# Performance work log

Measured on AMD Instinct MI355X. Metric: run time of the kernel, lower is better.

## Reference

```python
import jax, jax.numpy as jnp
from jax import lax
import numpy as np

REG = 0.1        # entropic regularization
ITERS = 50       # Sinkhorn iterations
DS = 8           # avg-pool downsample factor
EPS = 1e-8


def _avg_pool_scaled(x, d):
    # F.avg_pool2d(x, d) * d**2 == sum over non-overlapping dxd windows
    B, C, H, W = x.shape
    return x.reshape(B, C, H // d, d, W // d, d).mean(axis=(3, 5)) * (d * d)


def _cost_matrix(H, W):
    y = jnp.arange(H, dtype=jnp.float32)
    x = jnp.arange(W, dtype=jnp.float32)
    yy, xx = jnp.meshgrid(y, x, indexing='ij')
    coords = jnp.stack([yy.ravel(), xx.ravel()], axis=1)      # [N, 2]
    diff = coords[:, None, :] - coords[None, :, :]            # [N, N, 2]
    return (diff ** 2).sum(axis=-1)                           # [N, N] squared euclidean


def setup_inputs() -> dict:
    key = jax.random.key(0)
    k1, k2 = jax.random.split(key)
    B, H, W = 16, 512, 512
    pred_density = jax.random.uniform(k1, (B, 1, H, W), dtype=jnp.float32)
    gt_density = jax.random.uniform(k2, (B, 1, H, W), dtype=jnp.float32)
    return {"pred_density": pred_density, "gt_density": gt_density}


def reference(pred_density, gt_density):
    pred = _avg_pool_scaled(pred_density, DS)
    gt = _avg_pool_scaled(gt_density, DS)
    B, _, H, W = pred.shape
    N = H * W

    C = _cost_matrix(H, W)          # [N, N]
    K = jnp.exp(-C / REG)           # Gibbs kernel
    M = K * C                       # so cost = u @ (M @ v) == sum(P * C) without materializing P

    a = pred.reshape(B, N)
    b = gt.reshape(B, N)
    a_sum = jnp.clip(a.sum(axis=1), 1e-8, None)
    b_sum = jnp.clip(b.sum(axis=1), 1e-8, None)
    a_n = a / a_sum[:, None]
    b_n = b / b_sum[:, None]

    def sinkhorn_cost(a1, b1):
        def step(carry, _):
            u, v = carry
            v = b1 / (K.T @ u + EPS)
            u = a1 / (K @ v + EPS)
            return (u, v), None
        (u, v), _ = lax.scan(step, (jnp.ones_like(a1), jnp.zeros_like(b1)),
                             None, length=ITERS)
        # P = u[:,None] * K * v[None,:]; (P*C).sum() = u^T (K*C) v
        return u @ (M @ v)

    costs = jax.vmap(sinkhorn_cost)(a_n, b_n)                 # [B]
    valid = (a_sum > 0.5) & (b_sum > 0.5)
    return jnp.where(valid, costs, 0.0).sum() / B
```

## Files before the change

kernel.cpp:

```cpp
#include <hip/hip_runtime.h>


#define G1 4.5399929762484854e-05f
#define EPSF 1e-8f

__device__ __forceinline__ float dpp_shr1(float x) {
  return __int_as_float(__builtin_amdgcn_update_dpp(0, __float_as_int(x), 0x138, 0xF, 0xF, true));
}
__device__ __forceinline__ float dpp_shl1(float x) {
  return __int_as_float(__builtin_amdgcn_update_dpp(0, __float_as_int(x), 0x130, 0xF, 0xF, true));
}

extern "C" __global__ void __launch_bounds__(256)
ot_pool(const float* __restrict__ pred, const float* __restrict__ gt,
        float* __restrict__ ws_pool, double* __restrict__ ws_part) {
  const int bx    = blockIdx.x;
  const int batch = bx & 15;
  const int which = (bx >> 4) & 1;
  const int slice = bx >> 5;
  const float* src  = (which ? gt : pred) + batch * (512 * 512);
  float*       outp = ws_pool + which * (16 * 4096) + batch * 4096;

  double part = 0.0;
  for (int k = 0; k < 2; ++k) {
    const int wi = slice * 512 + k * 256 + threadIdx.x;
    const int y = wi >> 6, x = wi & 63;
    const float* base = src + (y * 8) * 512 + x * 8;
    float s = 0.f;
#pragma unroll
    for (int dy = 0; dy < 8; ++dy) {
      const float4* r4 = (const float4*)(base + dy * 512);
      float4 p0 = r4[0], p1 = r4[1];
      s += ((p0.x + p0.y) + (p0.z + p0.w)) + ((p1.x + p1.y) + (p1.z + p1.w));
    }
    outp[wi] = s;
    part += (double)s;
  }
#pragma unroll
  for (int off = 32; off > 0; off >>= 1) part += __shfl_down(part, off, 64);
  __shared__ double pr[4];
  if ((threadIdx.x & 63) == 0) pr[threadIdx.x >> 6] = part;
  __syncthreads();
  if (threadIdx.x == 0)
    ws_part[slice * 32 + which * 16 + batch] = (pr[0] + pr[1]) + (pr[2] + pr[3]);
}

__device__ __forceinline__ void halfpass(const float (&src)[16], float (&dst)[16],
                                         const float (&wt)[16],
                                         float (*bnd)[4][64], int wv, int lane) {
  float th[16];
#pragma unroll
  for (int r = 0; r < 16; ++r) {
    float l  = dpp_shr1(src[r]);
    float rr = dpp_shl1(src[r]);
    th[r] = __builtin_fmaf(G1, l + rr, src[r]);
  }
  bnd[0][wv][lane] = th[0];
  bnd[1][wv][lane] = th[15];
  __syncthreads();
  float up = (wv > 0) ? bnd[1][wv - 1][lane] : 0.0f;
  float dn = (wv < 3) ? bnd[0][wv + 1][lane] : 0.0f;
#pragma unroll
  for (int r = 1; r < 15; ++r) {
    float s = __builtin_fmaf(G1, th[r - 1] + th[r + 1], th[r]);
    dst[r] = wt[r] * __builtin_amdgcn_rcpf(s + EPSF);
  }
  float s0 = __builtin_fmaf(G1, up + th[1], th[0]);
  dst[0] = wt[0] * __builtin_amdgcn_rcpf(s0 + EPSF);
  float s15 = __builtin_fmaf(G1, th[14] + dn, th[15]);
  dst[15] = wt[15] * __builtin_amdgcn_rcpf(s15 + EPSF);
}

extern "C" __global__ void __launch_bounds__(256)
ot_sinkhorn(const float* __restrict__ ws_pool, const double* __restrict__ ws_part,
            float* __restrict__ ws_cost) {
  const int batch = blockIdx.x;
  const int lane  = threadIdx.x & 63;
  const int wv    = threadIdx.x >> 6;

  __shared__ float  bnd[2][2][4][64];
  __shared__ float  bnd2[4][4][64];
  __shared__ double sums_sh[2];
  __shared__ double red[4];

  if (threadIdx.x == 0) {
    double sa = 0.0, sb = 0.0;
    for (int s = 0; s < 8; ++s) {
      sa += ws_part[s * 32 + batch];
      sb += ws_part[s * 32 + 16 + batch];
    }
    sums_sh[0] = sa; sums_sh[1] = sb;
  }
  __syncthreads();
  const float a_sum = (float)sums_sh[0];
  const float b_sum = (float)sums_sh[1];
  const float inva = 1.0f / fmaxf(a_sum, 1e-8f);
  const float invb = 1.0f / fmaxf(b_sum, 1e-8f);

  float av[16], bv[16], u[16], v[16];
  const float* pa = ws_pool + batch * 4096;
  const float* pb = ws_pool + 16 * 4096 + batch * 4096;
#pragma unroll
  for (int r = 0; r < 16; ++r) {
    const int idx = (wv * 16 + r) * 64 + lane;
    av[r] = pa[idx] * inva;
    bv[r] = pb[idx] * invb;
    u[r]  = 1.0f;
  }

#pragma unroll 1
  for (int it = 0; it < 50; ++it) {
    halfpass(u, v, bv, bnd[0], wv, lane);
    halfpass(v, u, av, bnd[1], wv, lane);
  }

  float tg[16], th2[16];
#pragma unroll
  for (int r = 0; r < 16; ++r) {
    float sh = dpp_shr1(v[r]) + dpp_shl1(v[r]);
    tg[r]  = __builtin_fmaf(G1, sh, v[r]);
    th2[r] = G1 * sh;
  }
  bnd2[0][wv][lane] = tg[0];
  bnd2[1][wv][lane] = tg[15];
  bnd2[2][wv][lane] = th2[0];
  bnd2[3][wv][lane] = th2[15];
  __syncthreads();
  const float tg_up = (wv > 0) ? bnd2[1][wv - 1][lane] : 0.f;
  const float tg_dn = (wv < 3) ? bnd2[0][wv + 1][lane] : 0.f;
  const float th_up = (wv > 0) ? bnd2[3][wv - 1][lane] : 0.f;
  const float th_dn = (wv < 3) ? bnd2[2][wv + 1][lane] : 0.f;

  double acc = 0.0;
#pragma unroll
  for (int r = 0; r < 16; ++r) {
    const float tgm = (r == 0)  ? tg_up : tg[r - 1];
    const float tgp = (r == 15) ? tg_dn : tg[r + 1];
    const float thm = (r == 0)  ? th_up : th2[r - 1];
    const float thp = (r == 15) ? th_dn : th2[r + 1];
    const float mv = G1 * (tgm + tgp) + __builtin_fmaf(G1, thm + thp, th2[r]);
    acc += (double)(u[r] * mv);
  }
#pragma unroll
  for (int off = 32; off > 0; off >>= 1) acc += __shfl_down(acc, off, 64);
  if (lane == 0) red[wv] = acc;
  __syncthreads();
  if (threadIdx.x == 0) {
    const double c = (red[0] + red[1]) + (red[2] + red[3]);
    const bool valid = (a_sum > 0.5f) && (b_sum > 0.5f);
    ws_cost[batch] = valid ? (float)c : 0.0f;
  }
}

extern "C" __global__ void ot_final(const float* __restrict__ ws_cost,
                                    float* __restrict__ out) {
  if (threadIdx.x == 0 && blockIdx.x == 0) {
    double s = 0.0;
    for (int i = 0; i < 16; ++i) s += (double)ws_cost[i];
    out[0] = (float)(s / 16.0);
  }
}

extern "C" void kernel_launch(void* const* d_in, const int* in_sizes, int n_in,
                              void* d_out, int out_size, void* d_ws, size_t ws_size,
                              hipStream_t stream) {
  (void)in_sizes; (void)n_in; (void)out_size; (void)ws_size;
  const float* pred = (const float*)d_in[0];
  const float* gt   = (const float*)d_in[1];

  float*  ws_pool = (float*)d_ws;
  double* ws_part = (double*)((char*)d_ws + 2 * 16 * 4096 * 4);
  float*  ws_cost = (float*)((char*)d_ws + 2 * 16 * 4096 * 4 + 2048);

  hipLaunchKernelGGL(ot_pool,     dim3(256), dim3(256), 0, stream, pred, gt, ws_pool, ws_part);
  hipLaunchKernelGGL(ot_sinkhorn, dim3(16),  dim3(256), 0, stream, ws_pool, ws_part, ws_cost);
  hipLaunchKernelGGL(ot_final,    dim3(1),   dim3(64),  0, stream, ws_cost, (float*)d_out);
}
```

Measured before the change: 115.1 us.

## Restructure Sinkhorn stencil exchange and fold final reduction into atomic add

```diff
diff --git a/kernel.cpp b/kernel.cpp
--- a/kernel.cpp
+++ b/kernel.cpp
@@ -45,55 +45,56 @@
     ws_part[slice * 32 + which * 16 + batch] = (pr[0] + pr[1]) + (pr[2] + pr[3]);
 }
 
-__device__ __forceinline__ void halfpass(const float (&src)[16], float (&dst)[16],
-                                         const float (&wt)[16],
-                                         float (*bnd)[4][64], int wv, int lane) {
-  float th[16];
-#pragma unroll
-  for (int r = 0; r < 16; ++r) {
-    float l  = dpp_shr1(src[r]);
-    float rr = dpp_shl1(src[r]);
-    th[r] = __builtin_fmaf(G1, l + rr, src[r]);
-  }
-  bnd[0][wv][lane] = th[0];
-  bnd[1][wv][lane] = th[15];
-  __syncthreads();
-  float up = (wv > 0) ? bnd[1][wv - 1][lane] : 0.0f;
-  float dn = (wv < 3) ? bnd[0][wv + 1][lane] : 0.0f;
+__device__ __forceinline__ void ot_step(const float (&src)[16], float (&dst)[16],
+                                        const float (&wt)[16],
+                                        float (*rd)[6][64], float (*wr)[6][64],
+                                        int wv, int lane) {
+  const float up = rd[1][wv][lane];
+  const float dn = rd[0][wv + 2][lane];
 #pragma unroll
   for (int r = 1; r < 15; ++r) {
-    float s = __builtin_fmaf(G1, th[r - 1] + th[r + 1], th[r]);
-    dst[r] = wt[r] * __builtin_amdgcn_rcpf(s + EPSF);
+    const float s = (dpp_shr1(src[r]) + dpp_shl1(src[r])) + (src[r - 1] + src[r + 1]);
+    dst[r] = wt[r] * __builtin_amdgcn_rcpf(__builtin_fmaf(G1, s, src[r]) + EPSF);
   }
-  float s0 = __builtin_fmaf(G1, up + th[1], th[0]);
-  dst[0] = wt[0] * __builtin_amdgcn_rcpf(s0 + EPSF);
-  float s15 = __builtin_fmaf(G1, th[14] + dn, th[15]);
-  dst[15] = wt[15] * __builtin_amdgcn_rcpf(s15 + EPSF);
+  const float s0 = (dpp_shr1(src[0]) + dpp_shl1(src[0])) + (up + src[1]);
+  dst[0] = wt[0] * __builtin_amdgcn_rcpf(__builtin_fmaf(G1, s0, src[0]) + EPSF);
+  const float s15 = (dpp_shr1(src[15]) + dpp_shl1(src[15])) + (src[14] + dn);
+  dst[15] = wt[15] * __builtin_amdgcn_rcpf(__builtin_fmaf(G1, s15, src[15]) + EPSF);
+  wr[0][wv + 1][lane] = dst[0];
+  wr[1][wv + 1][lane] = dst[15];
+  __syncthreads();
 }
 
 extern "C" __global__ void __launch_bounds__(256)
 ot_sinkhorn(const float* __restrict__ ws_pool, const double* __restrict__ ws_part,
-            float* __restrict__ ws_cost) {
+            float* __restrict__ out) {
   const int batch = blockIdx.x;
   const int lane  = threadIdx.x & 63;
   const int wv    = threadIdx.x >> 6;
 
-  __shared__ float  bnd[2][2][4][64];
-  __shared__ float  bnd2[4][4][64];
-  __shared__ double sums_sh[2];
-  __shared__ double red[4];
+  __shared__ float  bnd[2][2][6][64];
+  __shared__ double ssh[2];
+  __shared__ float  red[4];
 
-  if (threadIdx.x == 0) {
-    double sa = 0.0, sb = 0.0;
-    for (int s = 0; s < 8; ++s) {
-      sa += ws_part[s * 32 + batch];
-      sb += ws_part[s * 32 + 16 + batch];
-    }
-    sums_sh[0] = sa; sums_sh[1] = sb;
+  double s = 0.0;
+  if (threadIdx.x < 16)
+    s = ws_part[(threadIdx.x & 7) * 32 + ((threadIdx.x & 8) ? 16 : 0) + batch];
+  s += __shfl_down(s, 4, 64);
+  s += __shfl_down(s, 2, 64);
+  s += __shfl_down(s, 1, 64);
+  if (threadIdx.x == 0) ssh[0] = s;
+  if (threadIdx.x == 8) ssh[1] = s;
+
+  bnd[0][0][wv + 1][lane] = 1.0f;
+  bnd[0][1][wv + 1][lane] = 1.0f;
+  if (wv == 0) {
+    bnd[0][1][0][lane] = 0.f; bnd[0][0][5][lane] = 0.f;
+    bnd[1][1][0][lane] = 0.f; bnd[1][0][5][lane] = 0.f;
   }
   __syncthreads();
-  const float a_sum = (float)sums_sh[0];
-  const float b_sum = (float)sums_sh[1];
+
+  const float a_sum = (float)ssh[0];
+  const float b_sum = (float)ssh[1];
   const float inva = 1.0f / fmaxf(a_sum, 1e-8f);
   const float invb = 1.0f / fmaxf(b_sum, 1e-8f);
 
@@ -110,54 +111,28 @@
 
 #pragma unroll 1
   for (int it = 0; it < 50; ++it) {
-    halfpass(u, v, bv, bnd[0], wv, lane);
-    halfpass(v, u, av, bnd[1], wv, lane);
+    ot_step(u, v, bv, bnd[0], bnd[1], wv, lane);
+    ot_step(v, u, av, bnd[1], bnd[0], wv, lane);
   }
 
-  float tg[16], th2[16];
+  const float up = bnd[1][1][wv][lane];
+  const float dn = bnd[1][0][wv + 2][lane];
+  float acc = 0.f;
 #pragma unroll
   for (int r = 0; r < 16; ++r) {
-    float sh = dpp_shr1(v[r]) + dpp_shl1(v[r]);
-    tg[r]  = __builtin_fmaf(G1, sh, v[r]);
-    th2[r] = G1 * sh;
-  }
-  bnd2[0][wv][lane] = tg[0];
-  bnd2[1][wv][lane] = tg[15];
-  bnd2[2][wv][lane] = th2[0];
-  bnd2[3][wv][lane] = th2[15];
-  __syncthreads();
-  const float tg_up = (wv > 0) ? bnd2[1][wv - 1][lane] : 0.f;
-  const float tg_dn = (wv < 3) ? bnd2[0][wv + 1][lane] : 0.f;
-  const float th_up = (wv > 0) ? bnd2[3][wv - 1][lane] : 0.f;
-  const float th_dn = (wv < 3) ? bnd2[2][wv + 1][lane] : 0.f;
-
-  double acc = 0.0;
-#pragma unroll
-  for (int r = 0; r < 16; ++r) {
-    const float tgm = (r == 0)  ? tg_up : tg[r - 1];
-    const float tgp = (r == 15) ? tg_dn : tg[r + 1];
-    const float thm = (r == 0)  ? th_up : th2[r - 1];
-    const float thp = (r == 15) ? th_dn : th2[r + 1];
-    const float mv = G1 * (tgm + tgp) + __builtin_fmaf(G1, thm + thp, th2[r]);
-    acc += (double)(u[r] * mv);
+    const float vm = (r == 0)  ? up : v[r - 1];
+    const float vp = (r == 15) ? dn : v[r + 1];
+    const float sN = (dpp_shr1(v[r]) + dpp_shl1(v[r])) + (vm + vp);
+    acc = __builtin_fmaf(u[r], sN, acc);
   }
 #pragma unroll
   for (int off = 32; off > 0; off >>= 1) acc += __shfl_down(acc, off, 64);
   if (lane == 0) red[wv] = acc;
   __syncthreads();
   if (threadIdx.x == 0) {
-    const double c = (red[0] + red[1]) + (red[2] + red[3]);
+    const float c = G1 * ((red[0] + red[1]) + (red[2] + red[3]));
     const bool valid = (a_sum > 0.5f) && (b_sum > 0.5f);
-    ws_cost[batch] = valid ? (float)c : 0.0f;
-  }
-}
-
-extern "C" __global__ void ot_final(const float* __restrict__ ws_cost,
-                                    float* __restrict__ out) {
-  if (threadIdx.x == 0 && blockIdx.x == 0) {
-    double s = 0.0;
-    for (int i = 0; i < 16; ++i) s += (double)ws_cost[i];
-    out[0] = (float)(s / 16.0);
+    if (valid) atomicAdd(out, c * (1.0f / 16.0f));
   }
 }
 
@@ -170,9 +145,7 @@
 
   float*  ws_pool = (float*)d_ws;
   double* ws_part = (double*)((char*)d_ws + 2 * 16 * 4096 * 4);
-  float*  ws_cost = (float*)((char*)d_ws + 2 * 16 * 4096 * 4 + 2048);
 
   hipLaunchKernelGGL(ot_pool,     dim3(256), dim3(256), 0, stream, pred, gt, ws_pool, ws_part);
-  hipLaunchKernelGGL(ot_sinkhorn, dim3(16),  dim3(256), 0, stream, ws_pool, ws_part, ws_cost);
-  hipLaunchKernelGGL(ot_final,    dim3(1),   dim3(64),  0, stream, ws_cost, (float*)d_out);
+  hipLaunchKernelGGL(ot_sinkhorn, dim3(16),  dim3(256), 0, stream, ws_pool, ws_part, (float*)d_out);
 }
```

After: 110.2 us. -4.2%, faster.
